# Kernel optimization log

Measured on AMD Instinct MI355X. Metric: run time of the kernel, lower is better.

Reference implementation:

```python
import jax, jax.numpy as jnp
import numpy as np

B = 16384
D = 1024          # in_features
R = 64            # low_rank
E = 4             # num_experts
L = 3             # layer_num


def setup_inputs() -> dict:
    key = jax.random.key(0)
    ks = jax.random.split(key, 6)
    # xavier-normal-ish scales
    s_uv = (2.0 / (D + R)) ** 0.5
    s_c = (2.0 / (R + R)) ** 0.5
    s_g = (2.0 / (D + 1)) ** 0.5
    return {
        "inputs": jax.random.normal(ks[0], (B, D), dtype=jnp.float32),
        "U": jax.random.normal(ks[1], (L, E, D, R), dtype=jnp.float32) * s_uv,
        "V": jax.random.normal(ks[2], (L, E, D, R), dtype=jnp.float32) * s_uv,
        "C": jax.random.normal(ks[3], (L, E, R, R), dtype=jnp.float32) * s_c,
        "gate_w": jax.random.normal(ks[4], (E, D), dtype=jnp.float32) * s_g,
        "bias": jnp.zeros((L, D), dtype=jnp.float32),
    }


def reference(inputs, U, V, C, gate_w, bias):
    x0 = inputs                                  # [B, D]
    x_l = x0
    for i in range(L):
        # gating: per-expert Linear(d,1) on x_l -> [B, E], softmax over experts
        gates = jax.nn.softmax(x_l @ gate_w.T, axis=1)        # [B, E]
        # v_x = tanh(V_e^T x_l) for all experts at once
        v = jnp.tanh(jnp.einsum('bd,edr->ber', x_l, V[i]))    # [B, E, R]
        v = jnp.tanh(jnp.einsum('ers,bes->ber', C[i], v))     # [B, E, R]
        uv = jnp.einsum('edr,ber->bed', U[i], v)              # [B, E, D]
        dot = x0[:, None, :] * (uv + bias[i][None, None, :])  # [B, E, D]
        moe_out = jnp.einsum('bed,be->bd', dot, gates)        # [B, D]
        x_l = moe_out + x_l
    return x_l
```

## Files before the change

### kernel.cpp

```cpp
#include <hip/hip_runtime.h>
#include <math.h>

#define BB 16384
#define DD 1024
#define RR 64
#define EE 4
#define ER 256
#define LL 3

#define LDM 72

typedef __bf16 bf16x8 __attribute__((ext_vector_type(8)));
typedef float f32x4 __attribute__((ext_vector_type(4)));
typedef unsigned short us;

static __device__ inline us f2b(float f) {
    union { float f; unsigned u; } c; c.f = f;
    return (us)((c.u + 0x7FFF + ((c.u >> 16) & 1)) >> 16);
}
static __device__ inline float b2f(us v) {
    union { unsigned u; float f; } c; c.u = ((unsigned)v) << 16;
    return c.f;
}
static __device__ inline float fast_tanh(float x) {
    float t = __expf(2.f * x);
    return 1.f - 2.f / (t + 1.f);
}
static __device__ __forceinline__ void ld_lds16(const us* g, us* l) {
    __builtin_amdgcn_global_load_lds((const __attribute__((address_space(1))) void*)g,
                                     (__attribute__((address_space(3))) void*)l, 16, 0, 0);
}

__global__ __launch_bounds__(256) void convF2B(const float* __restrict__ s, us* __restrict__ d) {
    int f = (blockIdx.x * 256 + threadIdx.x) * 4;
    float4 v = *(const float4*)&s[f];
    *(ushort4*)&d[f] = make_ushort4(f2b(v.x), f2b(v.y), f2b(v.z), f2b(v.w));
}
__global__ __launch_bounds__(256) void convV(const float* __restrict__ V, us* __restrict__ Vt) {
    const int le = blockIdx.x;
    const int d0 = blockIdx.y * 64;
    __shared__ float t[64 * 65];
    const int tid = threadIdx.x;
    const float* Vb = V + (size_t)le * DD * RR;
    #pragma unroll
    for (int p = 0; p < 4; ++p) {
        int f = tid + p * 256; int dd = f >> 4; int c = (f & 15) * 4;
        float4 v = *(const float4*)&Vb[(size_t)(d0 + dd) * RR + c];
        t[dd * 65 + c + 0] = v.x; t[dd * 65 + c + 1] = v.y;
        t[dd * 65 + c + 2] = v.z; t[dd * 65 + c + 3] = v.w;
    }
    __syncthreads();
    int r = tid >> 2, dg = (tid & 3) * 16;
    us o[16];
    #pragma unroll
    for (int k = 0; k < 16; ++k) o[k] = f2b(t[(dg + k) * 65 + r]);
    us* dst = Vt + (size_t)le * RR * DD + (size_t)r * DD + d0 + dg;
    #pragma unroll
    for (int q = 0; q < 4; ++q) *(ushort4*)&dst[q * 4] = *(ushort4*)&o[q * 4];
}

__global__ __launch_bounds__(256) void gemm1_fused(const us* __restrict__ xb,
                                                   const us* __restrict__ Vt,
                                                   const us* __restrict__ Ce,
                                                   const us* __restrict__ gwb,
                                                   us* __restrict__ w) {
    const int row0 = blockIdx.x * 64;
    const int tid = threadIdx.x;
    const int lane = tid & 63, wave = tid >> 6;
    const int l15 = lane & 15, quad = lane >> 4;
    const int e64 = wave * 64;

    __shared__ __align__(16) union {
        struct { us buf[2][10240]; us gw[4096]; float gates[256]; } s;
        us Tt[4][4608];
    } u;

    const int kcA = (lane & 3) ^ ((lane >> 3) & 3);
    const int sA  = quad ^ ((l15 >> 1) & 3);

    #pragma unroll
    for (int i = 0; i < 2; ++i)
        ld_lds16(gwb + (size_t)(lane & 3) * DD + (i * 64 + wave * 16 + (lane >> 2)) * 8,
                 &u.s.gw[(i * 256 + e64) * 8]);

    auto STAGE = [&](int bi, int k0) {
        us* bb = u.s.buf[bi];
        #pragma unroll
        for (int i = 0; i < 4; ++i) {
            int row = i * 64 + wave * 16 + (lane >> 2);
            ld_lds16(Vt + (size_t)row * DD + k0 + kcA * 8, &bb[i * 2048 + wave * 512]);
        }
        {
            int row = wave * 16 + (lane >> 2);
            ld_lds16(xb + (size_t)(row0 + row) * DD + k0 + kcA * 8, &bb[8192 + wave * 512]);
        }
    };

    f32x4 acc[4][4] = {};
    f32x4 accg = {};
    STAGE(0, 0);

    for (int t = 0; t < 32; ++t) {
        __builtin_amdgcn_s_barrier();
        if (t < 31) {
            STAGE((t + 1) & 1, (t + 1) * 32);
            asm volatile("s_waitcnt vmcnt(5)" ::: "memory");
        } else {
            asm volatile("s_waitcnt vmcnt(0)" ::: "memory");
        }
        __builtin_amdgcn_s_barrier();
        __builtin_amdgcn_sched_barrier(0);
        const us* bb = u.s.buf[t & 1];
        bf16x8 af[4], bfr[4];
        #pragma unroll
        for (int mt = 0; mt < 4; ++mt)
            af[mt] = *(const bf16x8*)&bb[(e64 + mt * 16 + l15) * 32 + sA * 8];
        #pragma unroll
        for (int nt = 0; nt < 4; ++nt)
            bfr[nt] = *(const bf16x8*)&bb[8192 + (nt * 16 + l15) * 32 + sA * 8];
        bf16x8 bfrg = *(const bf16x8*)&bb[8192 + (wave * 16 + l15) * 32 + sA * 8];
        bf16x8 afg  = *(const bf16x8*)&u.s.gw[(t * 4 + quad) * 32 + (l15 & 3) * 8];
        #pragma unroll
        for (int mt = 0; mt < 4; ++mt)
            #pragma unroll
            for (int nt = 0; nt < 4; ++nt)
                acc[mt][nt] = __builtin_amdgcn_mfma_f32_16x16x32_bf16(af[mt], bfr[nt], acc[mt][nt], 0, 0, 0);
        accg = __builtin_amdgcn_mfma_f32_16x16x32_bf16(afg, bfrg, accg, 0, 0, 0);
    }
    __builtin_amdgcn_s_barrier();

    us* Tt = u.Tt[wave];
    #pragma unroll
    for (int mt = 0; mt < 4; ++mt)
        #pragma unroll
        for (int nt = 0; nt < 4; ++nt) {
            int b = nt * 16 + l15;
            us o[4];
            #pragma unroll
            for (int i = 0; i < 4; ++i) o[i] = f2b(fast_tanh(acc[mt][nt][i]));
            *(ushort4*)&Tt[b * LDM + mt * 16 + quad * 4] = *(ushort4*)o;
        }
    if (quad == 0) {
        float l0 = accg[0], l1 = accg[1], l2 = accg[2], l3 = accg[3];
        float m = fmaxf(fmaxf(l0, l1), fmaxf(l2, l3));
        float g0 = __expf(l0 - m), g1 = __expf(l1 - m);
        float g2 = __expf(l2 - m), g3 = __expf(l3 - m);
        float inv = 1.f / (g0 + g1 + g2 + g3);
        int b = wave * 16 + l15;
        u.s.gates[0 * 64 + b] = g0 * inv; u.s.gates[1 * 64 + b] = g1 * inv;
        u.s.gates[2 * 64 + b] = g2 * inv; u.s.gates[3 * 64 + b] = g3 * inv;
    }
    __syncthreads();

    const us* Cb = Ce + (size_t)wave * RR * RR;
    f32x4 acc2[4][4] = {};
    #pragma unroll
    for (int ks = 0; ks < 2; ++ks) {
        bf16x8 af2[4], bf2[4];
        #pragma unroll
        for (int mt = 0; mt < 4; ++mt)
            af2[mt] = *(const bf16x8*)&Cb[(size_t)(mt * 16 + l15) * RR + ks * 32 + quad * 8];
        #pragma unroll
        for (int nt = 0; nt < 4; ++nt)
            bf2[nt] = *(const bf16x8*)&Tt[(nt * 16 + l15) * LDM + ks * 32 + quad * 8];
        #pragma unroll
        for (int mt = 0; mt < 4; ++mt)
            #pragma unroll
            for (int nt = 0; nt < 4; ++nt)
                acc2[mt][nt] = __builtin_amdgcn_mfma_f32_16x16x32_bf16(af2[mt], bf2[nt], acc2[mt][nt], 0, 0, 0);
    }
    #pragma unroll
    for (int mt = 0; mt < 4; ++mt)
        #pragma unroll
        for (int nt = 0; nt < 4; ++nt) {
            int b = nt * 16 + l15;
            float g = u.s.gates[e64 + b];
            us o[4];
            #pragma unroll
            for (int i = 0; i < 4; ++i) o[i] = f2b(g * fast_tanh(acc2[mt][nt][i]));
            *(ushort4*)&w[(size_t)(row0 + b) * ER + e64 + mt * 16 + quad * 4] = *(ushort4*)o;
        }
}

__global__ __launch_bounds__(512, 4) void gemm2_combine(const us* __restrict__ w,
                                                        const us* __restrict__ Ub,
                                                        const float* __restrict__ x0,
                                                        us* __restrict__ xb,
                                                        const float* __restrict__ biasl,
                                                        float* __restrict__ out, int last) {
    const int row0 = blockIdx.x * 128;
    const int d0 = blockIdx.y * 128;
    __shared__ __align__(16) us sm2[2][8192];
    const int tid = threadIdx.x;
    const int lane = tid & 63, wave = tid >> 6;
    const int bh = wave & 1, dh = wave >> 1;
    const int l15 = lane & 15, quad = lane >> 4;

    const int kcA = (lane & 3) ^ ((lane >> 3) & 3);
    const int sA  = quad ^ ((l15 >> 1) & 3);

    auto STAGE = [&](int bi, int s) {
        int e = s >> 1, r0q = (s & 1) * 32;
        us* bb = sm2[bi];
        int row = wave * 16 + (lane >> 2);
        ld_lds16(Ub + ((size_t)e * DD + d0 + row) * RR + r0q + kcA * 8, &bb[wave * 512]);
        ld_lds16(w + (size_t)(row0 + row) * ER + e * 64 + r0q + kcA * 8, &bb[4096 + wave * 512]);
    };

    f32x4 acc[2][4] = {};
    STAGE(0, 0);
    for (int t = 0; t < 8; ++t) {
        __builtin_amdgcn_s_barrier();
        if (t < 7) {
            STAGE((t + 1) & 1, t + 1);
            asm volatile("s_waitcnt vmcnt(2)" ::: "memory");
        } else {
            asm volatile("s_waitcnt vmcnt(0)" ::: "memory");
        }
        __builtin_amdgcn_s_barrier();
        __builtin_amdgcn_sched_barrier(0);
        const us* bb = sm2[t & 1];
        bf16x8 af[2], bfr[4];
        #pragma unroll
        for (int mt = 0; mt < 2; ++mt)
            af[mt] = *(const bf16x8*)&bb[(dh * 32 + mt * 16 + l15) * 32 + sA * 8];
        #pragma unroll
        for (int nt = 0; nt < 4; ++nt)
            bfr[nt] = *(const bf16x8*)&bb[4096 + (bh * 64 + nt * 16 + l15) * 32 + sA * 8];
        #pragma unroll
        for (int mt = 0; mt < 2; ++mt)
            #pragma unroll
            for (int nt = 0; nt < 4; ++nt)
                acc[mt][nt] = __builtin_amdgcn_mfma_f32_16x16x32_bf16(af[mt], bfr[nt], acc[mt][nt], 0, 0, 0);
    }

    float4 xv[2][4]; ushort4 xl[2][4];
    #pragma unroll
    for (int mt = 0; mt < 2; ++mt)
        #pragma unroll
        for (int nt = 0; nt < 4; ++nt) {
            size_t base = (size_t)(row0 + bh * 64 + nt * 16 + l15) * DD
                        + (d0 + dh * 32 + mt * 16 + quad * 4);
            xv[mt][nt] = *(const float4*)&x0[base];
            xl[mt][nt] = *(const ushort4*)&xb[base];
        }
    float4 bv[2];
    #pragma unroll
    for (int mt = 0; mt < 2; ++mt)
        bv[mt] = *(const float4*)&biasl[d0 + dh * 32 + mt * 16 + quad * 4];

    #pragma unroll
    for (int mt = 0; mt < 2; ++mt)
        #pragma unroll
        for (int nt = 0; nt < 4; ++nt) {
            size_t base = (size_t)(row0 + bh * 64 + nt * 16 + l15) * DD
                        + (d0 + dh * 32 + mt * 16 + quad * 4);
            float4 o;
            o.x = xv[mt][nt].x * (acc[mt][nt][0] + bv[mt].x) + b2f(xl[mt][nt].x);
            o.y = xv[mt][nt].y * (acc[mt][nt][1] + bv[mt].y) + b2f(xl[mt][nt].y);
            o.z = xv[mt][nt].z * (acc[mt][nt][2] + bv[mt].z) + b2f(xl[mt][nt].z);
            o.w = xv[mt][nt].w * (acc[mt][nt][3] + bv[mt].w) + b2f(xl[mt][nt].w);
            if (last) {
                *(float4*)&out[base] = o;
            } else {
                *(ushort4*)&xb[base] = make_ushort4(f2b(o.x), f2b(o.y), f2b(o.z), f2b(o.w));
            }
        }
}

extern "C" void kernel_launch(void* const* d_in, const int* in_sizes, int n_in,
                              void* d_out, int out_size, void* d_ws, size_t ws_size,
                              hipStream_t stream) {
    const float* inputs = (const float*)d_in[0];
    const float* U      = (const float*)d_in[1];
    const float* V      = (const float*)d_in[2];
    const float* C      = (const float*)d_in[3];
    const float* gw     = (const float*)d_in[4];
    const float* bias   = (const float*)d_in[5];
    float* out = (float*)d_out;

    us*    xb    = (us*)d_ws;
    us*    wbf   = xb + (size_t)BB * DD;
    float* gsc   = (float*)(wbf + (size_t)BB * ER);
    us*    gwb   = (us*)gsc;
    us*    Vt    = (us*)(gsc + (size_t)BB * 4);
    us*    Ub    = Vt + (size_t)LL * EE * RR * DD;
    us*    Cb    = Ub + (size_t)LL * EE * DD * RR;

    convF2B<<<dim3(BB * DD / 1024), 256, 0, stream>>>(inputs, xb);
    convF2B<<<dim3(LL * EE * DD * RR / 1024), 256, 0, stream>>>(U, Ub);
    convF2B<<<dim3(LL * EE * RR * RR / 1024), 256, 0, stream>>>(C, Cb);
    convF2B<<<dim3(EE * DD / 1024), 256, 0, stream>>>(gw, gwb);
    convV<<<dim3(LL * EE, DD / 64), 256, 0, stream>>>(V, Vt);

    for (int i = 0; i < LL; ++i) {
        gemm1_fused<<<dim3(BB / 64), 256, 0, stream>>>(
            xb, Vt + (size_t)i * EE * RR * DD, Cb + (size_t)i * EE * RR * RR, gwb, wbf);
        gemm2_combine<<<dim3(BB / 128, DD / 128), 512, 0, stream>>>(
            wbf, Ub + (size_t)i * EE * DD * RR, inputs, xb, bias + (size_t)i * DD,
            out, i == LL - 1);
    }
}
```

Baseline: 325.4 us.

## Deepen gemm1 pipeline with 8 waves; restage gemm2 epilogue through LDS with bf16 x0

gemm1 now runs 512 threads with the batch tile split across two wave halves and a 4-deep LDS ring (three stages in flight) in place of double buffering. gemm2's epilogue moves accumulators through swizzled LDS so each thread does wide coalesced 16-element loads and stores, and it reads x0 from a bf16 copy instead of fp32. These changes target load latency in gemm1 and uncoalesced, wide fp32 traffic in the combine step. The costs are more LDS per block and lower precision for x0 in the final product.

```diff
diff --git a/kernel.cpp b/kernel.cpp
--- a/kernel.cpp
+++ b/kernel.cpp
@@ -59,88 +59,93 @@
     for (int q = 0; q < 4; ++q) *(ushort4*)&dst[q * 4] = *(ushort4*)&o[q * 4];
 }
 
-__global__ __launch_bounds__(256) void gemm1_fused(const us* __restrict__ xb,
-                                                   const us* __restrict__ Vt,
-                                                   const us* __restrict__ Ce,
-                                                   const us* __restrict__ gwb,
-                                                   us* __restrict__ w) {
+__global__ __launch_bounds__(512, 2) void gemm1_fused(const us* __restrict__ xs,
+                                                      const us* __restrict__ Vt,
+                                                      const us* __restrict__ Ce,
+                                                      const us* __restrict__ gwb,
+                                                      us* __restrict__ w) {
     const int row0 = blockIdx.x * 64;
     const int tid = threadIdx.x;
     const int lane = tid & 63, wave = tid >> 6;
     const int l15 = lane & 15, quad = lane >> 4;
-    const int e64 = wave * 64;
+    const int e = wave & 3, h = wave >> 2;
+    const int e64 = e * 64;
 
     __shared__ __align__(16) union {
-        struct { us buf[2][10240]; us gw[4096]; float gates[256]; } s;
-        us Tt[4][4608];
+        struct { us buf[4][10240]; us gw[4096]; float gates[256]; } s;
+        us Tt[4][64 * LDM];
     } u;
 
-    const int kcA = (lane & 3) ^ ((lane >> 3) & 3);
-    const int sA  = quad ^ ((l15 >> 1) & 3);
-
-    #pragma unroll
-    for (int i = 0; i < 2; ++i)
-        ld_lds16(gwb + (size_t)(lane & 3) * DD + (i * 64 + wave * 16 + (lane >> 2)) * 8,
-                 &u.s.gw[(i * 256 + e64) * 8]);
+    const int kcA  = (lane & 3) ^ ((lane >> 3) & 3);
+    const int sA   = quad ^ ((l15 >> 1) & 3);
+    const int rsub = lane >> 2;
+
+    ld_lds16(gwb + (size_t)(lane & 3) * DD + (wave * 16 + rsub) * 8, &u.s.gw[wave * 512]);
 
     auto STAGE = [&](int bi, int k0) {
         us* bb = u.s.buf[bi];
         #pragma unroll
-        for (int i = 0; i < 4; ++i) {
-            int row = i * 64 + wave * 16 + (lane >> 2);
-            ld_lds16(Vt + (size_t)row * DD + k0 + kcA * 8, &bb[i * 2048 + wave * 512]);
-        }
-        {
-            int row = wave * 16 + (lane >> 2);
-            ld_lds16(xb + (size_t)(row0 + row) * DD + k0 + kcA * 8, &bb[8192 + wave * 512]);
+        for (int j = 0; j < 2; ++j) {
+            int row = wave * 32 + j * 16 + rsub;
+            ld_lds16(Vt + (size_t)row * DD + k0 + kcA * 8, &bb[(wave * 32 + j * 16) * 32]);
+        }
+        if (wave < 4) {
+            int row = wave * 16 + rsub;
+            ld_lds16(xs + (size_t)(row0 + row) * DD + k0 + kcA * 8, &bb[8192 + wave * 512]);
         }
     };
 
-    f32x4 acc[4][4] = {};
+    f32x4 acc[4][2] = {};
     f32x4 accg = {};
-    STAGE(0, 0);
+    STAGE(0, 0); STAGE(1, 32); STAGE(2, 64);
 
     for (int t = 0; t < 32; ++t) {
-        __builtin_amdgcn_s_barrier();
-        if (t < 31) {
-            STAGE((t + 1) & 1, (t + 1) * 32);
-            asm volatile("s_waitcnt vmcnt(5)" ::: "memory");
+        if (t < 30) {
+            if (wave < 4) asm volatile("s_waitcnt vmcnt(6)" ::: "memory");
+            else          asm volatile("s_waitcnt vmcnt(4)" ::: "memory");
+        } else if (t == 30) {
+            if (wave < 4) asm volatile("s_waitcnt vmcnt(3)" ::: "memory");
+            else          asm volatile("s_waitcnt vmcnt(2)" ::: "memory");
         } else {
             asm volatile("s_waitcnt vmcnt(0)" ::: "memory");
         }
         __builtin_amdgcn_s_barrier();
+        if (t < 29) STAGE((t + 3) & 3, (t + 3) * 32);
         __builtin_amdgcn_sched_barrier(0);
-        const us* bb = u.s.buf[t & 1];
-        bf16x8 af[4], bfr[4];
+        const us* bb = u.s.buf[t & 3];
+        bf16x8 af[4], bfr[2];
         #pragma unroll
         for (int mt = 0; mt < 4; ++mt)
             af[mt] = *(const bf16x8*)&bb[(e64 + mt * 16 + l15) * 32 + sA * 8];
         #pragma unroll
-        for (int nt = 0; nt < 4; ++nt)
-            bfr[nt] = *(const bf16x8*)&bb[8192 + (nt * 16 + l15) * 32 + sA * 8];
-        bf16x8 bfrg = *(const bf16x8*)&bb[8192 + (wave * 16 + l15) * 32 + sA * 8];
-        bf16x8 afg  = *(const bf16x8*)&u.s.gw[(t * 4 + quad) * 32 + (l15 & 3) * 8];
+        for (int nt = 0; nt < 2; ++nt)
+            bfr[nt] = *(const bf16x8*)&bb[8192 + (h * 32 + nt * 16 + l15) * 32 + sA * 8];
         #pragma unroll
         for (int mt = 0; mt < 4; ++mt)
             #pragma unroll
-            for (int nt = 0; nt < 4; ++nt)
+            for (int nt = 0; nt < 2; ++nt)
                 acc[mt][nt] = __builtin_amdgcn_mfma_f32_16x16x32_bf16(af[mt], bfr[nt], acc[mt][nt], 0, 0, 0);
-        accg = __builtin_amdgcn_mfma_f32_16x16x32_bf16(afg, bfrg, accg, 0, 0, 0);
+        if (wave < 4) {
+            bf16x8 bfrg = *(const bf16x8*)&bb[8192 + (wave * 16 + l15) * 32 + sA * 8];
+            bf16x8 afg  = *(const bf16x8*)&u.s.gw[(t * 4 + quad) * 32 + (l15 & 3) * 8];
+            accg = __builtin_amdgcn_mfma_f32_16x16x32_bf16(afg, bfrg, accg, 0, 0, 0);
+        }
     }
     __builtin_amdgcn_s_barrier();
-
-    us* Tt = u.Tt[wave];
+    __builtin_amdgcn_sched_barrier(0);
+
+    us* Tt = u.Tt[e];
     #pragma unroll
     for (int mt = 0; mt < 4; ++mt)
         #pragma unroll
-        for (int nt = 0; nt < 4; ++nt) {
-            int b = nt * 16 + l15;
+        for (int nt = 0; nt < 2; ++nt) {
+            int b = h * 32 + nt * 16 + l15;
             us o[4];
             #pragma unroll
             for (int i = 0; i < 4; ++i) o[i] = f2b(fast_tanh(acc[mt][nt][i]));
             *(ushort4*)&Tt[b * LDM + mt * 16 + quad * 4] = *(ushort4*)o;
         }
-    if (quad == 0) {
+    if (wave < 4 && quad == 0) {
         float l0 = accg[0], l1 = accg[1], l2 = accg[2], l3 = accg[3];
         float m = fmaxf(fmaxf(l0, l1), fmaxf(l2, l3));
         float g0 = __expf(l0 - m), g1 = __expf(l1 - m);
@@ -152,28 +157,28 @@
     }
     __syncthreads();
 
-    const us* Cb = Ce + (size_t)wave * RR * RR;
-    f32x4 acc2[4][4] = {};
+    const us* Cb = Ce + (size_t)e * RR * RR;
+    f32x4 acc2[4][2] = {};
     #pragma unroll
     for (int ks = 0; ks < 2; ++ks) {
-        bf16x8 af2[4], bf2[4];
+        bf16x8 af2[4], bf2[2];
         #pragma unroll
         for (int mt = 0; mt < 4; ++mt)
             af2[mt] = *(const bf16x8*)&Cb[(size_t)(mt * 16 + l15) * RR + ks * 32 + quad * 8];
         #pragma unroll
-        for (int nt = 0; nt < 4; ++nt)
-            bf2[nt] = *(const bf16x8*)&Tt[(nt * 16 + l15) * LDM + ks * 32 + quad * 8];
+        for (int nt = 0; nt < 2; ++nt)
+            bf2[nt] = *(const bf16x8*)&Tt[(h * 32 + nt * 16 + l15) * LDM + ks * 32 + quad * 8];
         #pragma unroll
         for (int mt = 0; mt < 4; ++mt)
             #pragma unroll
-            for (int nt = 0; nt < 4; ++nt)
+            for (int nt = 0; nt < 2; ++nt)
                 acc2[mt][nt] = __builtin_amdgcn_mfma_f32_16x16x32_bf16(af2[mt], bf2[nt], acc2[mt][nt], 0, 0, 0);
     }
     #pragma unroll
     for (int mt = 0; mt < 4; ++mt)
         #pragma unroll
-        for (int nt = 0; nt < 4; ++nt) {
-            int b = nt * 16 + l15;
+        for (int nt = 0; nt < 2; ++nt) {
+            int b = h * 32 + nt * 16 + l15;
             float g = u.s.gates[e64 + b];
             us o[4];
             #pragma unroll
@@ -184,13 +189,14 @@
 
 __global__ __launch_bounds__(512, 4) void gemm2_combine(const us* __restrict__ w,
                                                         const us* __restrict__ Ub,
-                                                        const float* __restrict__ x0,
-                                                        us* __restrict__ xb,
+                                                        const us* __restrict__ x0b,
+                                                        const us* __restrict__ xls,
+                                                        us* __restrict__ xbo,
                                                         const float* __restrict__ biasl,
                                                         float* __restrict__ out, int last) {
     const int row0 = blockIdx.x * 128;
     const int d0 = blockIdx.y * 128;
-    __shared__ __align__(16) us sm2[2][8192];
+    __shared__ __align__(16) union { us stage[2][8192]; float smf[8192]; } su;
     const int tid = threadIdx.x;
     const int lane = tid & 63, wave = tid >> 6;
     const int bh = wave & 1, dh = wave >> 1;
@@ -201,7 +207,7 @@
 
     auto STAGE = [&](int bi, int s) {
         int e = s >> 1, r0q = (s & 1) * 32;
-        us* bb = sm2[bi];
+        us* bb = su.stage[bi];
         int row = wave * 16 + (lane >> 2);
         ld_lds16(Ub + ((size_t)e * DD + d0 + row) * RR + r0q + kcA * 8, &bb[wave * 512]);
         ld_lds16(w + (size_t)(row0 + row) * ER + e * 64 + r0q + kcA * 8, &bb[4096 + wave * 512]);
@@ -219,7 +225,7 @@
         }
         __builtin_amdgcn_s_barrier();
         __builtin_amdgcn_sched_barrier(0);
-        const us* bb = sm2[t & 1];
+        const us* bb = su.stage[t & 1];
         bf16x8 af[2], bfr[4];
         #pragma unroll
         for (int mt = 0; mt < 2; ++mt)
@@ -234,38 +240,62 @@
                 acc[mt][nt] = __builtin_amdgcn_mfma_f32_16x16x32_bf16(af[mt], bfr[nt], acc[mt][nt], 0, 0, 0);
     }
 
-    float4 xv[2][4]; ushort4 xl[2][4];
-    #pragma unroll
-    for (int mt = 0; mt < 2; ++mt)
-        #pragma unroll
-        for (int nt = 0; nt < 4; ++nt) {
-            size_t base = (size_t)(row0 + bh * 64 + nt * 16 + l15) * DD
-                        + (d0 + dh * 32 + mt * 16 + quad * 4);
-            xv[mt][nt] = *(const float4*)&x0[base];
-            xl[mt][nt] = *(const ushort4*)&xb[base];
-        }
-    float4 bv[2];
-    #pragma unroll
-    for (int mt = 0; mt < 2; ++mt)
-        bv[mt] = *(const float4*)&biasl[d0 + dh * 32 + mt * 16 + quad * 4];
-
-    #pragma unroll
-    for (int mt = 0; mt < 2; ++mt)
-        #pragma unroll
-        for (int nt = 0; nt < 4; ++nt) {
-            size_t base = (size_t)(row0 + bh * 64 + nt * 16 + l15) * DD
-                        + (d0 + dh * 32 + mt * 16 + quad * 4);
-            float4 o;
-            o.x = xv[mt][nt].x * (acc[mt][nt][0] + bv[mt].x) + b2f(xl[mt][nt].x);
-            o.y = xv[mt][nt].y * (acc[mt][nt][1] + bv[mt].y) + b2f(xl[mt][nt].y);
-            o.z = xv[mt][nt].z * (acc[mt][nt][2] + bv[mt].z) + b2f(xl[mt][nt].z);
-            o.w = xv[mt][nt].w * (acc[mt][nt][3] + bv[mt].w) + b2f(xl[mt][nt].w);
-            if (last) {
-                *(float4*)&out[base] = o;
-            } else {
-                *(ushort4*)&xb[base] = make_ushort4(f2b(o.x), f2b(o.y), f2b(o.z), f2b(o.w));
+    const int erow = tid >> 2;
+    const int ec   = tid & 3;
+    const size_t gb = (size_t)(row0 + erow) * DD + d0;
+    #pragma unroll
+    for (int p = 0; p < 2; ++p) {
+        const int doff = p * 64 + ec * 16;
+        uint xu[8], lu[8];
+        *(uint4*)&xu[0] = *(const uint4*)&x0b[gb + doff];
+        *(uint4*)&xu[4] = *(const uint4*)&x0b[gb + doff + 8];
+        *(uint4*)&lu[0] = *(const uint4*)&xls[gb + doff];
+        *(uint4*)&lu[4] = *(const uint4*)&xls[gb + doff + 8];
+        float bf[16];
+        *(float4*)&bf[0]  = *(const float4*)&biasl[d0 + doff];
+        *(float4*)&bf[4]  = *(const float4*)&biasl[d0 + doff + 4];
+        *(float4*)&bf[8]  = *(const float4*)&biasl[d0 + doff + 8];
+        *(float4*)&bf[12] = *(const float4*)&biasl[d0 + doff + 12];
+        __syncthreads();
+        if ((dh >> 1) == p) {
+            #pragma unroll
+            for (int mt = 0; mt < 2; ++mt)
+                #pragma unroll
+                for (int nt = 0; nt < 4; ++nt) {
+                    int r = bh * 64 + nt * 16 + l15;
+                    int s = (dh & 1) * 8 + mt * 4 + quad;
+                    *(f32x4*)&su.smf[r * 64 + ((s ^ (r & 15)) << 2)] = acc[mt][nt];
+                }
+        }
+        __syncthreads();
+        float o[16];
+        #pragma unroll
+        for (int j = 0; j < 4; ++j) {
+            int s = ec * 4 + j;
+            float4 a = *(const float4*)&su.smf[erow * 64 + ((s ^ (erow & 15)) << 2)];
+            #pragma unroll
+            for (int i = 0; i < 4; ++i) {
+                int k = j * 4 + i;
+                float av = (i == 0) ? a.x : (i == 1) ? a.y : (i == 2) ? a.z : a.w;
+                uint uu = xu[k >> 1], ll = lu[k >> 1];
+                float xv = b2f((k & 1) ? (us)(uu >> 16) : (us)(uu & 0xffff));
+                float xl = b2f((k & 1) ? (us)(ll >> 16) : (us)(ll & 0xffff));
+                o[k] = xv * (av + bf[k]) + xl;
             }
         }
+        if (last) {
+            *(float4*)&out[gb + doff]      = *(float4*)&o[0];
+            *(float4*)&out[gb + doff + 4]  = *(float4*)&o[4];
+            *(float4*)&out[gb + doff + 8]  = *(float4*)&o[8];
+            *(float4*)&out[gb + doff + 12] = *(float4*)&o[12];
+        } else {
+            us ob[16];
+            #pragma unroll
+            for (int k = 0; k < 16; ++k) ob[k] = f2b(o[k]);
+            *(uint4*)&xbo[gb + doff]     = *(uint4*)&ob[0];
+            *(uint4*)&xbo[gb + doff + 8] = *(uint4*)&ob[8];
+        }
+    }
 }
 
 extern "C" void kernel_launch(void* const* d_in, const int* in_sizes, int n_in,
@@ -279,25 +309,26 @@
     const float* bias   = (const float*)d_in[5];
     float* out = (float*)d_out;
 
-    us*    xb    = (us*)d_ws;
-    us*    wbf   = xb + (size_t)BB * DD;
-    float* gsc   = (float*)(wbf + (size_t)BB * ER);
-    us*    gwb   = (us*)gsc;
-    us*    Vt    = (us*)(gsc + (size_t)BB * 4);
-    us*    Ub    = Vt + (size_t)LL * EE * RR * DD;
-    us*    Cb    = Ub + (size_t)LL * EE * DD * RR;
-
-    convF2B<<<dim3(BB * DD / 1024), 256, 0, stream>>>(inputs, xb);
+    us* xb0 = (us*)d_ws;
+    us* xb  = xb0 + (size_t)BB * DD;
+    us* wbf = xb + (size_t)BB * DD;
+    us* gwb = wbf + (size_t)BB * ER;
+    us* Vt  = gwb + (size_t)EE * DD;
+    us* Ub  = Vt + (size_t)LL * EE * RR * DD;
+    us* Cb  = Ub + (size_t)LL * EE * DD * RR;
+
+    convF2B<<<dim3(BB * DD / 1024), 256, 0, stream>>>(inputs, xb0);
     convF2B<<<dim3(LL * EE * DD * RR / 1024), 256, 0, stream>>>(U, Ub);
     convF2B<<<dim3(LL * EE * RR * RR / 1024), 256, 0, stream>>>(C, Cb);
     convF2B<<<dim3(EE * DD / 1024), 256, 0, stream>>>(gw, gwb);
     convV<<<dim3(LL * EE, DD / 64), 256, 0, stream>>>(V, Vt);
 
     for (int i = 0; i < LL; ++i) {
-        gemm1_fused<<<dim3(BB / 64), 256, 0, stream>>>(
-            xb, Vt + (size_t)i * EE * RR * DD, Cb + (size_t)i * EE * RR * RR, gwb, wbf);
+        const us* xs = (i == 0) ? xb0 : xb;
+        gemm1_fused<<<dim3(BB / 64), 512, 0, stream>>>(
+            xs, Vt + (size_t)i * EE * RR * DD, Cb + (size_t)i * EE * RR * RR, gwb, wbf);
         gemm2_combine<<<dim3(BB / 128, DD / 128), 512, 0, stream>>>(
-            wbf, Ub + (size_t)i * EE * DD * RR, inputs, xb, bias + (size_t)i * DD,
+            wbf, Ub + (size_t)i * EE * DD * RR, xb0, xs, xb, bias + (size_t)i * DD,
             out, i == LL - 1);
     }
 }
```

New measurement: 279.1 us. 1.17x faster.
